# Kernel tuning notes

Measured on AMD Instinct MI355X. Metric: run time of the kernel, lower is better.

Reference implementation:

```python
import jax, jax.numpy as jnp
import numpy as np

B, LC, LQ, D = 32, 2048, 256, 256


def setup_inputs() -> dict:
    key = jax.random.key(0)
    kc, kq, kcm, kqm, kw = jax.random.split(key, 5)
    context = jax.random.normal(kc, (B, LC, D), dtype=jnp.float32)
    query = jax.random.normal(kq, (B, LQ, D), dtype=jnp.float32)
    # True = masked (matches torch masked_fill semantics)
    context_mask = jax.random.randint(kcm, (B, LC), 0, 2).astype(bool)
    query_mask = jax.random.randint(kqm, (B, LQ), 0, 2).astype(bool)
    # nn.Linear(3*dim, 1, bias=False) weight, flattened to (3D,)
    w0 = jax.random.normal(kw, (3 * D,), dtype=jnp.float32) * (1.0 / np.sqrt(3 * D))
    return {"context": context, "query": query, "context_mask": context_mask,
            "query_mask": query_mask, "w0": w0}


def reference(context, query, context_mask, query_mask, w0):
    d = context.shape[-1]
    wc, wq, wm = w0[:d], w0[d:2 * d], w0[2 * d:]
    # trilinear sim: w0 . [c, q, c*q]  ==  c.wc + q.wq + (c*wm) q^T
    sc = context @ wc                                   # (B, Lc)
    sq = query @ wq                                     # (B, Lq)
    sim = sc[:, :, None] + sq[:, None, :] + jnp.einsum(
        'bcd,bqd->bcq', context * wm, query)            # (B, Lc, Lq)
    mask = context_mask[:, :, None] | query_mask[:, None, :]
    sim = jnp.where(mask, jnp.float32(-1e30), sim)
    S = jax.nn.softmax(sim, axis=-1)                    # row softmax over Lq
    SS = jax.nn.softmax(sim, axis=1)                    # col softmax over Lc
    S = jnp.nan_to_num(S)
    SS = jnp.nan_to_num(SS)
    A = jnp.einsum('bcq,bqd->bcd', S, query)            # (B, Lc, D)
    T = jnp.einsum('bkq,bkd->bqd', SS, context)         # SS^T @ context, (B, Lq, D)
    Bmat = jnp.einsum('bcq,bqd->bcd', S, T)             # (B, Lc, D)
    return (A, Bmat)
```

## Files before the change

kernel.cpp:

```cpp
#include <hip/hip_runtime.h>

#define B_  32
#define LC_ 2048
#define LQ_ 256
#define D_  256
#define NEGH (-30000.0f)

typedef _Float16 f16;
typedef _Float16 f16x4 __attribute__((ext_vector_type(4)));
typedef _Float16 f16x8 __attribute__((ext_vector_type(8)));
typedef float    f32x4 __attribute__((ext_vector_type(4)));

__global__ __launch_bounds__(256) void k_prep(
    const float* __restrict__ ctx, const float* __restrict__ qry,
    const float* __restrict__ w0, f16* __restrict__ ctx16,
    f16* __restrict__ qrywm16, float* __restrict__ sc, float* __restrict__ sq)
{
    const int lane = threadIdx.x & 63;
    const int wave = threadIdx.x >> 6;
    const int row  = blockIdx.x * 4 + wave;
    const int NC = B_ * LC_;
    if (row < NC) {
        float4 v = *(const float4*)(ctx + (long long)row * D_ + lane * 4);
        f16x4 h; h[0] = (f16)v.x; h[1] = (f16)v.y; h[2] = (f16)v.z; h[3] = (f16)v.w;
        *(f16x4*)(ctx16 + (long long)row * D_ + lane * 4) = h;
        float4 wc = *(const float4*)(w0 + lane * 4);
        float s = v.x*wc.x + v.y*wc.y + v.z*wc.z + v.w*wc.w;
        #pragma unroll
        for (int off = 32; off > 0; off >>= 1) s += __shfl_down(s, off, 64);
        if (lane == 0) sc[row] = s;
    } else {
        int r = row - NC;
        float4 v = *(const float4*)(qry + (long long)r * D_ + lane * 4);
        float4 wm = *(const float4*)(w0 + 2 * D_ + lane * 4);
        f16x4 h;
        h[0] = (f16)(v.x * wm.x); h[1] = (f16)(v.y * wm.y);
        h[2] = (f16)(v.z * wm.z); h[3] = (f16)(v.w * wm.w);
        *(f16x4*)(qrywm16 + (long long)r * D_ + lane * 4) = h;
        float4 wq = *(const float4*)(w0 + D_ + lane * 4);
        float s = v.x*wq.x + v.y*wq.y + v.z*wq.z + v.w*wq.w;
        #pragma unroll
        for (int off = 32; off > 0; off >>= 1) s += __shfl_down(s, off, 64);
        if (lane == 0) sq[r] = s;
    }
}

__global__ __launch_bounds__(256) void k_tq(
    const float* __restrict__ in, f16* __restrict__ out)
{
    __shared__ float tile[64 * 65];
    const int b = blockIdx.z;
    const int r0 = blockIdx.x * 64, c0 = blockIdx.y * 64;
    const int t = threadIdx.x;
    const float* ib = in + (long long)b * LQ_ * D_;
    #pragma unroll
    for (int p = 0; p < 4; ++p) {
        int r = (t >> 4) + p * 16;
        int cb = (t & 15) * 4;
        float4 v = *(const float4*)(ib + (long long)(r0 + r) * D_ + c0 + cb);
        tile[r * 65 + cb + 0] = v.x;
        tile[r * 65 + cb + 1] = v.y;
        tile[r * 65 + cb + 2] = v.z;
        tile[r * 65 + cb + 3] = v.w;
    }
    __syncthreads();
    f16* ob = out + (long long)b * 512 * LQ_;
    #pragma unroll
    for (int p = 0; p < 4; ++p) {
        int c = (t >> 4) + p * 16;
        int rb = (t & 15) * 4;
        f16x4 h;
        h[0] = (f16)tile[(rb + 0) * 65 + c];
        h[1] = (f16)tile[(rb + 1) * 65 + c];
        h[2] = (f16)tile[(rb + 2) * 65 + c];
        h[3] = (f16)tile[(rb + 3) * 65 + c];
        *(f16x4*)(ob + (long long)(c0 + c) * LQ_ + r0 + rb) = h;
    }
}

#define LDA1 40
__global__ __launch_bounds__(256) void k_g1(
    const f16* __restrict__ ctx16, const f16* __restrict__ qrywm16,
    const float* __restrict__ sc, const float* __restrict__ sq,
    const int* __restrict__ cmask, const int* __restrict__ qmask,
    f16* __restrict__ sim16)
{
    __shared__ f16 As[128 * LDA1];
    __shared__ f16 Bs[256 * LDA1];
    const int b = blockIdx.z;
    const int c0 = blockIdx.x * 128;
    const int t = threadIdx.x, lane = t & 63, wv = t >> 6;
    const int wm_off = (wv >> 1) * 64, wn_off = (wv & 1) * 128;
    const f16* Ab = ctx16 + ((long long)b * LC_ + c0) * D_;
    const f16* Bb = qrywm16 + (long long)b * LQ_ * D_;
    const int srow = t >> 2, scg = (t & 3) * 8;
    f32x4 acc[4][8] = {};
    for (int k0 = 0; k0 < D_; k0 += 32) {
        #pragma unroll
        for (int p = 0; p < 2; ++p) {
            int r = srow + p * 64;
            *(f16x8*)(As + r * LDA1 + scg) = *(const f16x8*)(Ab + (long long)r * D_ + k0 + scg);
        }
        #pragma unroll
        for (int p = 0; p < 4; ++p) {
            int r = srow + p * 64;
            *(f16x8*)(Bs + r * LDA1 + scg) = *(const f16x8*)(Bb + (long long)r * D_ + k0 + scg);
        }
        __syncthreads();
        f16x8 af[4], bf[8];
        #pragma unroll
        for (int i = 0; i < 4; ++i)
            af[i] = *(const f16x8*)(As + (wm_off + i * 16 + (lane & 15)) * LDA1 + (lane >> 4) * 8);
        #pragma unroll
        for (int j = 0; j < 8; ++j)
            bf[j] = *(const f16x8*)(Bs + (wn_off + j * 16 + (lane & 15)) * LDA1 + (lane >> 4) * 8);
        #pragma unroll
        for (int i = 0; i < 4; ++i)
            #pragma unroll
            for (int j = 0; j < 8; ++j)
                acc[i][j] = __builtin_amdgcn_mfma_f32_16x16x32_f16(af[i], bf[j], acc[i][j], 0, 0, 0);
        __syncthreads();
    }
    float sqv[8]; int qmv[8];
    #pragma unroll
    for (int j = 0; j < 8; ++j) {
        int q = wn_off + j * 16 + (lane & 15);
        sqv[j] = sq[b * LQ_ + q];
        qmv[j] = qmask[b * LQ_ + q];
    }
    #pragma unroll
    for (int i = 0; i < 4; ++i) {
        #pragma unroll
        for (int r = 0; r < 4; ++r) {
            int c = c0 + wm_off + i * 16 + (lane >> 4) * 4 + r;
            float scv = sc[b * LC_ + c];
            int cm = cmask[b * LC_ + c];
            f16* orow = sim16 + ((long long)b * LC_ + c) * LQ_ + wn_off + (lane & 15);
            #pragma unroll
            for (int j = 0; j < 8; ++j) {
                float val = (cm | qmv[j]) ? NEGH : (acc[i][j][r] + scv + sqv[j]);
                orow[j * 16] = (f16)val;
            }
        }
    }
}

__global__ __launch_bounds__(256) void k_s1(
    const f16* __restrict__ sim16, float* __restrict__ rowm, float* __restrict__ rowinvl,
    float* __restrict__ pm, float* __restrict__ pl)
{
    __shared__ float tile[32 * 260];
    const int ch = blockIdx.x;
    const int b  = blockIdx.y;
    const int t  = threadIdx.x;
    const int c0 = ch * 32;
    const f16* sb = sim16 + ((long long)b * LC_ + c0) * LQ_;
    #pragma unroll
    for (int p = 0; p < 8; ++p) {
        int r = p * 4 + (t >> 6);
        int cb = (t & 63) * 4;
        f16x4 v = *(const f16x4*)(sb + (long long)r * LQ_ + cb);
        tile[r * 260 + cb + 0] = (float)v[0];
        tile[r * 260 + cb + 1] = (float)v[1];
        tile[r * 260 + cb + 2] = (float)v[2];
        tile[r * 260 + cb + 3] = (float)v[3];
    }
    __syncthreads();
    {
        int r = t >> 3, s = t & 7;
        const float* rp = tile + r * 260;
        float m = -INFINITY;
        #pragma unroll
        for (int i = 0; i < 32; ++i) m = fmaxf(m, rp[(i << 3) + s]);
        m = fmaxf(m, __shfl_xor(m, 1, 64));
        m = fmaxf(m, __shfl_xor(m, 2, 64));
        m = fmaxf(m, __shfl_xor(m, 4, 64));
        float l = 0.f;
        #pragma unroll
        for (int i = 0; i < 32; ++i) l += __expf(rp[(i << 3) + s] - m);
        l += __shfl_xor(l, 1, 64);
        l += __shfl_xor(l, 2, 64);
        l += __shfl_xor(l, 4, 64);
        if (s == 0) {
            rowm[b * LC_ + c0 + r] = m;
            rowinvl[b * LC_ + c0 + r] = 1.0f / l;
        }
    }
    {
        float m = -INFINITY;
        #pragma unroll 8
        for (int r = 0; r < 32; ++r) m = fmaxf(m, tile[r * 260 + t]);
        float l = 0.f;
        #pragma unroll 8
        for (int r = 0; r < 32; ++r) l += __expf(tile[r * 260 + t] - m);
        int idx = (b * 64 + ch) * LQ_ + t;
        pm[idx] = m; pl[idx] = l;
    }
}

__global__ __launch_bounds__(256) void k_colreduce(
    const float* __restrict__ pm, const float* __restrict__ pl,
    float* __restrict__ colm, float* __restrict__ colinvl)
{
    const int col = blockIdx.x * 256 + threadIdx.x;
    const int b = col >> 8, q = col & 255;
    float M = -INFINITY, L = 0.f;
    for (int ch = 0; ch < 64; ++ch) {
        int idx = (b * 64 + ch) * LQ_ + q;
        float m = pm[idx], l = pl[idx];
        float nM = fmaxf(M, m);
        L = L * __expf(M - nM) + l * __expf(m - nM);
        M = nM;
    }
    colm[col] = M; colinvl[col] = 1.0f / L;
}

#define LDA3 66
__global__ __launch_bounds__(256) void k_g3(
    const f16* __restrict__ ctx16, const f16* __restrict__ sim16,
    const float* __restrict__ colm, const float* __restrict__ colinvl,
    f16* __restrict__ Bcat)
{
    __shared__ f16 As[128 * LDA3];
    __shared__ f16 Bs[64 * LDA3];
    __shared__ float colm_s[64], cil_s[64];
    const int b = blockIdx.x;
    const int combo = blockIdx.y;
    const int qt = combo & 3, dh = combo >> 2;
    const int q0 = qt * 64, d0 = dh * 128;
    const int t = threadIdx.x, lane = t & 63, wv = t >> 6;
    const int wm_off = (wv >> 1) * 64, wn_off = (wv & 1) * 32;
    if (t < 64) {
        colm_s[t] = colm[b * LQ_ + q0 + t];
        cil_s[t]  = colinvl[b * LQ_ + q0 + t];
    }
    __syncthreads();
    const f16* Ab = ctx16 + (long long)b * LC_ * D_;
    const f16* Sb = sim16 + (long long)b * LC_ * LQ_;
    f32x4 acc[4][2] = {};
    const int acc_ = t >> 4, ad8 = (t & 15) * 8;
    const int bcc = t >> 3, bq8 = (t & 7) * 8;
    for (int c0 = 0; c0 < LC_; c0 += 64) {
        #pragma unroll
        for (int p = 0; p < 4; ++p) {
            int cc = acc_ + p * 16;
            f16x8 h = *(const f16x8*)(Ab + (long long)(c0 + cc) * D_ + d0 + ad8);
            #pragma unroll
            for (int j = 0; j < 8; ++j)
                As[(ad8 + j) * LDA3 + cc] = h[j];
        }
        #pragma unroll
        for (int p = 0; p < 2; ++p) {
            int cc = bcc + p * 32;
            f16x8 h = *(const f16x8*)(Sb + (long long)(c0 + cc) * LQ_ + q0 + bq8);
            #pragma unroll
            for (int j = 0; j < 8; ++j)
                Bs[(bq8 + j) * LDA3 + cc] = (f16)__expf((float)h[j] - colm_s[bq8 + j]);
        }
        __syncthreads();
        #pragma unroll
        for (int kk = 0; kk < 64; kk += 32) {
            f16x8 af[4], bf[2];
            #pragma unroll
            for (int i = 0; i < 4; ++i)
                af[i] = *(const f16x8*)(As + (wm_off + i * 16 + (lane & 15)) * LDA3 + kk + (lane >> 4) * 8);
            #pragma unroll
            for (int j = 0; j < 2; ++j)
                bf[j] = *(const f16x8*)(Bs + (wn_off + j * 16 + (lane & 15)) * LDA3 + kk + (lane >> 4) * 8);
            #pragma unroll
            for (int i = 0; i < 4; ++i)
                #pragma unroll
                for (int j = 0; j < 2; ++j)
                    acc[i][j] = __builtin_amdgcn_mfma_f32_16x16x32_f16(af[i], bf[j], acc[i][j], 0, 0, 0);
        }
        __syncthreads();
    }
    #pragma unroll
    for (int i = 0; i < 4; ++i) {
        #pragma unroll
        for (int r = 0; r < 4; ++r) {
            int d = d0 + wm_off + i * 16 + (lane >> 4) * 4 + r;
            f16* orow = Bcat + (long long)b * 512 * LQ_ + (long long)(256 + d) * LQ_ + q0 + wn_off + (lane & 15);
            #pragma unroll
            for (int j = 0; j < 2; ++j)
                orow[j * 16] = (f16)(acc[i][j][r] * cil_s[wn_off + j * 16 + (lane & 15)]);
        }
    }
}

__global__ __launch_bounds__(256) void k_g23(
    const f16* __restrict__ sim16, const float* __restrict__ rowm,
    const float* __restrict__ rowinvl, const f16* __restrict__ Bcat,
    float* __restrict__ outA, float* __restrict__ outB)
{
    __shared__ f16 As[128 * LDA1];
    __shared__ f16 Bs[128 * LDA1];
    const int b = blockIdx.z;
    const int c0 = blockIdx.x * 128, n0 = blockIdx.y * 128;
    const int t = threadIdx.x, lane = t & 63, wv = t >> 6;
    const int wm_off = (wv >> 1) * 64, wn_off = (wv & 1) * 64;
    const f16* Ab = sim16 + ((long long)b * LC_ + c0) * LQ_;
    const f16* Bb = Bcat + ((long long)b * 512 + n0) * LQ_;
    const int srow = t >> 2, scg = (t & 3) * 8;
    float rm[2];
    #pragma unroll
    for (int p = 0; p < 2; ++p) rm[p] = rowm[b * LC_ + c0 + srow + p * 64];
    f32x4 acc[4][4] = {};
    for (int k0 = 0; k0 < LQ_; k0 += 32) {
        #pragma unroll
        for (int p = 0; p < 2; ++p) {
            int r = srow + p * 64;
            f16x8 h = *(const f16x8*)(Ab + (long long)r * LQ_ + k0 + scg);
            f16x8 e;
            #pragma unroll
            for (int j = 0; j < 8; ++j) e[j] = (f16)__expf((float)h[j] - rm[p]);
            *(f16x8*)(As + r * LDA1 + scg) = e;
            *(f16x8*)(Bs + r * LDA1 + scg) = *(const f16x8*)(Bb + (long long)r * LQ_ + k0 + scg);
        }
        __syncthreads();
        f16x8 af[4], bf[4];
        #pragma unroll
        for (int i = 0; i < 4; ++i)
            af[i] = *(const f16x8*)(As + (wm_off + i * 16 + (lane & 15)) * LDA1 + (lane >> 4) * 8);
        #pragma unroll
        for (int j = 0; j < 4; ++j)
            bf[j] = *(const f16x8*)(Bs + (wn_off + j * 16 + (lane & 15)) * LDA1 + (lane >> 4) * 8);
        #pragma unroll
        for (int i = 0; i < 4; ++i)
            #pragma unroll
            for (int j = 0; j < 4; ++j)
                acc[i][j] = __builtin_amdgcn_mfma_f32_16x16x32_f16(af[i], bf[j], acc[i][j], 0, 0, 0);
        __syncthreads();
    }
    float* outp = (n0 < 256) ? outA : outB;
    const int nbase = (n0 < 256) ? n0 : (n0 - 256);
    #pragma unroll
    for (int i = 0; i < 4; ++i) {
        #pragma unroll
        for (int r = 0; r < 4; ++r) {
            int c = c0 + wm_off + i * 16 + (lane >> 4) * 4 + r;
            float ri = rowinvl[b * LC_ + c];
            float* orow = outp + ((long long)b * LC_ + c) * D_ + nbase + wn_off + (lane & 15);
            #pragma unroll
            for (int j = 0; j < 4; ++j)
                orow[j * 16] = acc[i][j][r] * ri;
        }
    }
}

extern "C" void kernel_launch(void* const* d_in, const int* in_sizes, int n_in,
                              void* d_out, int out_size, void* d_ws, size_t ws_size,
                              hipStream_t stream) {
    const float* ctx   = (const float*)d_in[0];
    const float* qry   = (const float*)d_in[1];
    const int*   cmask = (const int*)d_in[2];
    const int*   qmask = (const int*)d_in[3];
    const float* w0    = (const float*)d_in[4];
    float* out = (float*)d_out;

    char* w = (char*)d_ws;
    float* sc      = (float*)w;  w += (long long)65536 * 4;
    float* sq      = (float*)w;  w += (long long)8192 * 4;
    float* rowm    = (float*)w;  w += (long long)65536 * 4;
    float* rowinvl = (float*)w;  w += (long long)65536 * 4;
    float* colm    = (float*)w;  w += (long long)8192 * 4;
    float* colinvl = (float*)w;  w += (long long)8192 * 4;
    float* pm      = (float*)w;  w += (long long)524288 * 4;
    float* pl      = (float*)w;  w += (long long)524288 * 4;
    f16*   sim16   = (f16*)w;    w += (long long)16777216 * 2;
    f16*   ctx16   = (f16*)w;    w += (long long)16777216 * 2;
    f16*   qrywm16 = (f16*)w;    w += (long long)2097152 * 2;
    f16*   Bcat    = (f16*)w;    w += (long long)4194304 * 2;

    k_prep<<<18432, 256, 0, stream>>>(ctx, qry, w0, ctx16, qrywm16, sc, sq);
    k_tq<<<dim3(4, 4, 32), 256, 0, stream>>>(qry, Bcat);
    k_g1<<<dim3(16, 1, 32), 256, 0, stream>>>(ctx16, qrywm16, sc, sq, cmask, qmask, sim16);
    k_s1<<<dim3(64, 32), 256, 0, stream>>>(sim16, rowm, rowinvl, pm, pl);
    k_colreduce<<<32, 256, 0, stream>>>(pm, pl, colm, colinvl);
    k_g3<<<dim3(32, 8), 256, 0, stream>>>(ctx16, sim16, colm, colinvl, Bcat);
    k_g23<<<dim3(16, 4, 32), 256, 0, stream>>>(sim16, rowm, rowinvl, Bcat,
        out, out + (long long)B_ * LC_ * D_);
}
```

Baseline: 327.3 us.

## Fuse sim GEMM with row/column softmax stats; restructure output GEMM without LDS

```diff
diff --git a/kernel.cpp b/kernel.cpp
--- a/kernel.cpp
+++ b/kernel.cpp
@@ -78,124 +78,116 @@
     }
 }
 
-#define LDA1 40
-__global__ __launch_bounds__(256) void k_g1(
+__global__ __launch_bounds__(256) void k_f1(
     const f16* __restrict__ ctx16, const f16* __restrict__ qrywm16,
     const float* __restrict__ sc, const float* __restrict__ sq,
     const int* __restrict__ cmask, const int* __restrict__ qmask,
-    f16* __restrict__ sim16)
-{
-    __shared__ f16 As[128 * LDA1];
-    __shared__ f16 Bs[256 * LDA1];
-    const int b = blockIdx.z;
-    const int c0 = blockIdx.x * 128;
+    f16* __restrict__ sim16, float* __restrict__ rowm_g, float* __restrict__ rowinvl_g,
+    float* __restrict__ pm, float* __restrict__ pl)
+{
+    __shared__ f16 Bs[256 * 40];
+    const int b = blockIdx.y, c0 = blockIdx.x * 128;
     const int t = threadIdx.x, lane = t & 63, wv = t >> 6;
-    const int wm_off = (wv >> 1) * 64, wn_off = (wv & 1) * 128;
-    const f16* Ab = ctx16 + ((long long)b * LC_ + c0) * D_;
+    const int l15 = lane & 15, quad = lane >> 4;
+    const int wm = wv * 32;
+    const f16* Ab = ctx16 + ((long long)b * LC_ + c0 + wm) * D_;
     const f16* Bb = qrywm16 + (long long)b * LQ_ * D_;
-    const int srow = t >> 2, scg = (t & 3) * 8;
-    f32x4 acc[4][8] = {};
+    f32x4 acc[2][16] = {};
     for (int k0 = 0; k0 < D_; k0 += 32) {
         #pragma unroll
-        for (int p = 0; p < 2; ++p) {
-            int r = srow + p * 64;
-            *(f16x8*)(As + r * LDA1 + scg) = *(const f16x8*)(Ab + (long long)r * D_ + k0 + scg);
-        }
-        #pragma unroll
-        for (int p = 0; p < 4; ++p) {
-            int r = srow + p * 64;
-            *(f16x8*)(Bs + r * LDA1 + scg) = *(const f16x8*)(Bb + (long long)r * D_ + k0 + scg);
-        }
+        for (int g = 0; g < 4; ++g)
+            *(f16x8*)(Bs + t * 40 + g * 8) = *(const f16x8*)(Bb + (long long)t * D_ + k0 + g * 8);
+        f16x8 af[2];
+        #pragma unroll
+        for (int i = 0; i < 2; ++i)
+            af[i] = *(const f16x8*)(Ab + (long long)(i * 16 + l15) * D_ + k0 + quad * 8);
         __syncthreads();
-        f16x8 af[4], bf[8];
-        #pragma unroll
-        for (int i = 0; i < 4; ++i)
-            af[i] = *(const f16x8*)(As + (wm_off + i * 16 + (lane & 15)) * LDA1 + (lane >> 4) * 8);
-        #pragma unroll
-        for (int j = 0; j < 8; ++j)
-            bf[j] = *(const f16x8*)(Bs + (wn_off + j * 16 + (lane & 15)) * LDA1 + (lane >> 4) * 8);
-        #pragma unroll
-        for (int i = 0; i < 4; ++i)
-            #pragma unroll
-            for (int j = 0; j < 8; ++j)
-                acc[i][j] = __builtin_amdgcn_mfma_f32_16x16x32_f16(af[i], bf[j], acc[i][j], 0, 0, 0);
+        #pragma unroll
+        for (int j = 0; j < 16; ++j) {
+            f16x8 bf = *(const f16x8*)(Bs + (j * 16 + l15) * 40 + quad * 8);
+            acc[0][j] = __builtin_amdgcn_mfma_f32_16x16x32_f16(af[0], bf, acc[0][j], 0, 0, 0);
+            acc[1][j] = __builtin_amdgcn_mfma_f32_16x16x32_f16(af[1], bf, acc[1][j], 0, 0, 0);
+        }
         __syncthreads();
     }
-    float sqv[8]; int qmv[8];
-    #pragma unroll
-    for (int j = 0; j < 8; ++j) {
-        int q = wn_off + j * 16 + (lane & 15);
+    float scv[8]; int cmv[8];
+    #pragma unroll
+    for (int i = 0; i < 2; ++i)
+        #pragma unroll
+        for (int r = 0; r < 4; ++r) {
+            int c = c0 + wm + i * 16 + quad * 4 + r;
+            scv[i * 4 + r] = sc[b * LC_ + c];
+            cmv[i * 4 + r] = cmask[b * LC_ + c];
+        }
+    float sqv[16]; int qmv[16];
+    #pragma unroll
+    for (int j = 0; j < 16; ++j) {
+        int q = j * 16 + l15;
         sqv[j] = sq[b * LQ_ + q];
         qmv[j] = qmask[b * LQ_ + q];
     }
     #pragma unroll
-    for (int i = 0; i < 4; ++i) {
-        #pragma unroll
-        for (int r = 0; r < 4; ++r) {
-            int c = c0 + wm_off + i * 16 + (lane >> 4) * 4 + r;
-            float scv = sc[b * LC_ + c];
-            int cm = cmask[b * LC_ + c];
-            f16* orow = sim16 + ((long long)b * LC_ + c) * LQ_ + wn_off + (lane & 15);
-            #pragma unroll
-            for (int j = 0; j < 8; ++j) {
-                float val = (cm | qmv[j]) ? NEGH : (acc[i][j][r] + scv + sqv[j]);
-                orow[j * 16] = (f16)val;
+    for (int i = 0; i < 2; ++i)
+        #pragma unroll
+        for (int j = 0; j < 16; ++j)
+            #pragma unroll
+            for (int r = 0; r < 4; ++r) {
+                float v = acc[i][j][r] + scv[i * 4 + r] + sqv[j];
+                acc[i][j][r] = (cmv[i * 4 + r] | qmv[j]) ? NEGH : v;
             }
-        }
-    }
-}
-
-__global__ __launch_bounds__(256) void k_s1(
-    const f16* __restrict__ sim16, float* __restrict__ rowm, float* __restrict__ rowinvl,
-    float* __restrict__ pm, float* __restrict__ pl)
-{
-    __shared__ float tile[32 * 260];
-    const int ch = blockIdx.x;
-    const int b  = blockIdx.y;
-    const int t  = threadIdx.x;
-    const int c0 = ch * 32;
-    const f16* sb = sim16 + ((long long)b * LC_ + c0) * LQ_;
-    #pragma unroll
-    for (int p = 0; p < 8; ++p) {
-        int r = p * 4 + (t >> 6);
-        int cb = (t & 63) * 4;
-        f16x4 v = *(const f16x4*)(sb + (long long)r * LQ_ + cb);
-        tile[r * 260 + cb + 0] = (float)v[0];
-        tile[r * 260 + cb + 1] = (float)v[1];
-        tile[r * 260 + cb + 2] = (float)v[2];
-        tile[r * 260 + cb + 3] = (float)v[3];
-    }
-    __syncthreads();
-    {
-        int r = t >> 3, s = t & 7;
-        const float* rp = tile + r * 260;
+    #pragma unroll
+    for (int i = 0; i < 2; ++i)
+        #pragma unroll
+        for (int r = 0; r < 4; ++r) {
+            f16* orow = sim16 + ((long long)b * LC_ + c0 + wm + i * 16 + quad * 4 + r) * LQ_ + l15;
+            #pragma unroll
+            for (int j = 0; j < 16; ++j) orow[j * 16] = (f16)acc[i][j][r];
+        }
+    #pragma unroll
+    for (int j = 0; j < 16; ++j) {
         float m = -INFINITY;
         #pragma unroll
-        for (int i = 0; i < 32; ++i) m = fmaxf(m, rp[(i << 3) + s]);
-        m = fmaxf(m, __shfl_xor(m, 1, 64));
-        m = fmaxf(m, __shfl_xor(m, 2, 64));
-        m = fmaxf(m, __shfl_xor(m, 4, 64));
+        for (int i = 0; i < 2; ++i)
+            #pragma unroll
+            for (int r = 0; r < 4; ++r) m = fmaxf(m, acc[i][j][r]);
+        m = fmaxf(m, __shfl_xor(m, 16, 64));
+        m = fmaxf(m, __shfl_xor(m, 32, 64));
         float l = 0.f;
         #pragma unroll
-        for (int i = 0; i < 32; ++i) l += __expf(rp[(i << 3) + s] - m);
-        l += __shfl_xor(l, 1, 64);
-        l += __shfl_xor(l, 2, 64);
-        l += __shfl_xor(l, 4, 64);
-        if (s == 0) {
-            rowm[b * LC_ + c0 + r] = m;
-            rowinvl[b * LC_ + c0 + r] = 1.0f / l;
-        }
-    }
-    {
-        float m = -INFINITY;
-        #pragma unroll 8
-        for (int r = 0; r < 32; ++r) m = fmaxf(m, tile[r * 260 + t]);
-        float l = 0.f;
-        #pragma unroll 8
-        for (int r = 0; r < 32; ++r) l += __expf(tile[r * 260 + t] - m);
-        int idx = (b * 64 + ch) * LQ_ + t;
-        pm[idx] = m; pl[idx] = l;
-    }
+        for (int i = 0; i < 2; ++i)
+            #pragma unroll
+            for (int r = 0; r < 4; ++r) l += __expf(acc[i][j][r] - m);
+        l += __shfl_xor(l, 16, 64);
+        l += __shfl_xor(l, 32, 64);
+        if (quad == 0) {
+            int idx = (b * 64 + blockIdx.x * 4 + wv) * LQ_ + j * 16 + l15;
+            pm[idx] = m; pl[idx] = l;
+        }
+    }
+    #pragma unroll
+    for (int i = 0; i < 2; ++i)
+        #pragma unroll
+        for (int r = 0; r < 4; ++r) {
+            float m = -INFINITY;
+            #pragma unroll
+            for (int j = 0; j < 16; ++j) m = fmaxf(m, acc[i][j][r]);
+            m = fmaxf(m, __shfl_xor(m, 1, 64));
+            m = fmaxf(m, __shfl_xor(m, 2, 64));
+            m = fmaxf(m, __shfl_xor(m, 4, 64));
+            m = fmaxf(m, __shfl_xor(m, 8, 64));
+            float l = 0.f;
+            #pragma unroll
+            for (int j = 0; j < 16; ++j) l += __expf(acc[i][j][r] - m);
+            l += __shfl_xor(l, 1, 64);
+            l += __shfl_xor(l, 2, 64);
+            l += __shfl_xor(l, 4, 64);
+            l += __shfl_xor(l, 8, 64);
+            if (l15 == 0) {
+                int c = c0 + wm + i * 16 + quad * 4 + r;
+                rowm_g[b * LC_ + c] = m;
+                rowinvl_g[b * LC_ + c] = 1.0f / l;
+            }
+        }
 }
 
 __global__ __launch_bounds__(256) void k_colreduce(
@@ -288,64 +280,51 @@
     }
 }
 
-__global__ __launch_bounds__(256) void k_g23(
+__global__ __launch_bounds__(256) void k_f45(
     const f16* __restrict__ sim16, const float* __restrict__ rowm,
     const float* __restrict__ rowinvl, const f16* __restrict__ Bcat,
     float* __restrict__ outA, float* __restrict__ outB)
 {
-    __shared__ f16 As[128 * LDA1];
-    __shared__ f16 Bs[128 * LDA1];
-    const int b = blockIdx.z;
-    const int c0 = blockIdx.x * 128, n0 = blockIdx.y * 128;
+    const int b = blockIdx.y, c0 = blockIdx.x * 64;
     const int t = threadIdx.x, lane = t & 63, wv = t >> 6;
-    const int wm_off = (wv >> 1) * 64, wn_off = (wv & 1) * 64;
-    const f16* Ab = sim16 + ((long long)b * LC_ + c0) * LQ_;
-    const f16* Bb = Bcat + ((long long)b * 512 + n0) * LQ_;
-    const int srow = t >> 2, scg = (t & 3) * 8;
-    float rm[2];
-    #pragma unroll
-    for (int p = 0; p < 2; ++p) rm[p] = rowm[b * LC_ + c0 + srow + p * 64];
-    f32x4 acc[4][4] = {};
+    const int l15 = lane & 15, quad = lane >> 4;
+    const int ch = (wv >> 1) * 32;
+    const int nh = wv & 1;
+    const f16* Ab = sim16 + ((long long)b * LC_ + c0 + ch) * LQ_;
+    const f16* Bb = Bcat + ((long long)b * 512 + nh * 256) * LQ_;
+    float rm2[2];
+    #pragma unroll
+    for (int i = 0; i < 2; ++i)
+        rm2[i] = rowm[b * LC_ + c0 + ch + i * 16 + l15];
+    f32x4 acc[2][16] = {};
     for (int k0 = 0; k0 < LQ_; k0 += 32) {
-        #pragma unroll
-        for (int p = 0; p < 2; ++p) {
-            int r = srow + p * 64;
-            f16x8 h = *(const f16x8*)(Ab + (long long)r * LQ_ + k0 + scg);
-            f16x8 e;
-            #pragma unroll
-            for (int j = 0; j < 8; ++j) e[j] = (f16)__expf((float)h[j] - rm[p]);
-            *(f16x8*)(As + r * LDA1 + scg) = e;
-            *(f16x8*)(Bs + r * LDA1 + scg) = *(const f16x8*)(Bb + (long long)r * LQ_ + k0 + scg);
-        }
-        __syncthreads();
-        f16x8 af[4], bf[4];
-        #pragma unroll
-        for (int i = 0; i < 4; ++i)
-            af[i] = *(const f16x8*)(As + (wm_off + i * 16 + (lane & 15)) * LDA1 + (lane >> 4) * 8);
-        #pragma unroll
-        for (int j = 0; j < 4; ++j)
-            bf[j] = *(const f16x8*)(Bs + (wn_off + j * 16 + (lane & 15)) * LDA1 + (lane >> 4) * 8);
-        #pragma unroll
-        for (int i = 0; i < 4; ++i)
-            #pragma unroll
-            for (int j = 0; j < 4; ++j)
-                acc[i][j] = __builtin_amdgcn_mfma_f32_16x16x32_f16(af[i], bf[j], acc[i][j], 0, 0, 0);
-        __syncthreads();
-    }
-    float* outp = (n0 < 256) ? outA : outB;
-    const int nbase = (n0 < 256) ? n0 : (n0 - 256);
-    #pragma unroll
-    for (int i = 0; i < 4; ++i) {
-        #pragma unroll
-        for (int r = 0; r < 4; ++r) {
-            int c = c0 + wm_off + i * 16 + (lane >> 4) * 4 + r;
+        f16x8 af[2];
+        #pragma unroll
+        for (int i = 0; i < 2; ++i) {
+            f16x8 s8 = *(const f16x8*)(Ab + (long long)(i * 16 + l15) * LQ_ + k0 + quad * 8);
+            #pragma unroll
+            for (int jj = 0; jj < 8; ++jj)
+                af[i][jj] = (f16)__expf((float)s8[jj] - rm2[i]);
+        }
+        #pragma unroll
+        for (int j = 0; j < 16; ++j) {
+            f16x8 bf = *(const f16x8*)(Bb + (long long)(j * 16 + l15) * LQ_ + k0 + quad * 8);
+            acc[0][j] = __builtin_amdgcn_mfma_f32_16x16x32_f16(af[0], bf, acc[0][j], 0, 0, 0);
+            acc[1][j] = __builtin_amdgcn_mfma_f32_16x16x32_f16(af[1], bf, acc[1][j], 0, 0, 0);
+        }
+    }
+    float* outp = nh ? outB : outA;
+    #pragma unroll
+    for (int i = 0; i < 2; ++i)
+        #pragma unroll
+        for (int r = 0; r < 4; ++r) {
+            int c = c0 + ch + i * 16 + quad * 4 + r;
             float ri = rowinvl[b * LC_ + c];
-            float* orow = outp + ((long long)b * LC_ + c) * D_ + nbase + wn_off + (lane & 15);
-            #pragma unroll
-            for (int j = 0; j < 4; ++j)
+            float* orow = outp + ((long long)b * LC_ + c) * D_ + l15;
+            #pragma unroll
+            for (int j = 0; j < 16; ++j)
                 orow[j * 16] = acc[i][j][r] * ri;
         }
-    }
 }
 
 extern "C" void kernel_launch(void* const* d_in, const int* in_sizes, int n_in,
@@ -374,10 +353,10 @@
 
     k_prep<<<18432, 256, 0, stream>>>(ctx, qry, w0, ctx16, qrywm16, sc, sq);
     k_tq<<<dim3(4, 4, 32), 256, 0, stream>>>(qry, Bcat);
-    k_g1<<<dim3(16, 1, 32), 256, 0, stream>>>(ctx16, qrywm16, sc, sq, cmask, qmask, sim16);
-    k_s1<<<dim3(64, 32), 256, 0, stream>>>(sim16, rowm, rowinvl, pm, pl);
+    k_f1<<<dim3(16, 32), 256, 0, stream>>>(ctx16, qrywm16, sc, sq, cmask, qmask,
+        sim16, rowm, rowinvl, pm, pl);
     k_colreduce<<<32, 256, 0, stream>>>(pm, pl, colm, colinvl);
     k_g3<<<dim3(32, 8), 256, 0, stream>>>(ctx16, sim16, colm, colinvl, Bcat);
-    k_g23<<<dim3(16, 4, 32), 256, 0, stream>>>(sim16, rowm, rowinvl, Bcat,
+    k_f45<<<dim3(32, 32), 256, 0, stream>>>(sim16, rowm, rowinvl, Bcat,
         out, out + (long long)B_ * LC_ * D_);
 }
```

New measurement: 370.0 us. 13.0% more time.
